# Optimization experiments

Measured on AMD Instinct MI355X. Metric: run time of the kernel, lower is better.

Reference implementation:

```python
import jax, jax.numpy as jnp
import numpy as np

B, ME, R, N, HSZ, V, L, NHEADS = 32, 384, 128, 512, 500, 1000, 2, 4


def _ln(x, g, b, eps=1e-5):
    mu = jnp.mean(x, axis=-1, keepdims=True)
    var = jnp.mean((x - mu) ** 2, axis=-1, keepdims=True)
    return (x - mu) / jnp.sqrt(var + eps) * g + b


def setup_inputs() -> dict:
    key = jax.random.key(0)
    ks = jax.random.split(key, 12)
    ent_vec = jax.random.normal(ks[0], (B, ME, HSZ), jnp.float32)
    entity_num = jax.random.randint(ks[1], (B,), 1, ME + 1)
    rels = jax.random.randint(ks[2], (B, R), 0, V)
    sizes = entity_num + R  # real graph size per sample (<= N)
    idx = jnp.arange(N)
    valid = idx[None, :] < sizes[:, None]
    adj = jax.random.uniform(ks[3], (B, N, N)) < 0.3
    adj = adj & valid[:, None, :] & valid[:, :, None]
    adj = adj | jnp.eye(N, dtype=bool)[None]  # keep diagonal so no all-masked row
    adj = adj.astype(jnp.int32)
    rel_embed = jax.random.normal(ks[4], (V, HSZ)) * (2.0 / (V + HSZ)) ** 0.5  # xavier_normal

    def w(k, shape):
        return (jax.random.normal(k, shape) * 0.03).astype(jnp.float32)

    Wq = w(ks[5], (L, HSZ, HSZ)); Wk = w(ks[6], (L, HSZ, HSZ))
    Wv = w(ks[7], (L, HSZ, HSZ)); Wo = w(ks[8], (L, HSZ, HSZ))
    W1 = w(ks[9], (L, HSZ, 4 * HSZ)); W2 = w(ks[10], (L, 4 * HSZ, HSZ))
    zH = jnp.zeros((L, HSZ), jnp.float32)
    return dict(
        ent_vec=ent_vec, entity_num=entity_num, rels=rels, adj=adj,
        rel_embed=rel_embed,
        Wq=Wq, bq=zH, Wk=Wk, bk=zH, Wv=Wv, bv=zH, Wo=Wo, bo=zH,
        W1=W1, b1=jnp.zeros((L, 4 * HSZ), jnp.float32), W2=W2, b2=zH,
        ln1_g=jnp.ones((L, HSZ), jnp.float32), ln1_b=zH,
        ln2_g=jnp.ones((L, HSZ), jnp.float32), ln2_b=zH,
        prelu_a=jnp.full((L, 4 * HSZ), 0.25, jnp.float32),
    )


def reference(ent_vec, entity_num, rels, adj, rel_embed,
              Wq, bq, Wk, bk, Wv, bv, Wo, bo,
              W1, b1, W2, b2, ln1_g, ln1_b, ln2_g, ln2_b, prelu_a):
    Bb, Me, H = ent_vec.shape
    Rr = rels.shape[1]
    Nn = adj.shape[1]
    Ll = Wq.shape[0]
    dh = H // NHEADS
    idx = jnp.arange(Nn)

    # query_graph = concat(ent_vec[i][:entity_num[i]], rel_embed(rels[i])), padded to N
    is_ent = idx[None, :] < entity_num[:, None]
    eidx = jnp.minimum(idx[None, :], Me - 1)
    ent_part = jnp.take_along_axis(ent_vec, eidx[:, :, None], axis=1)  # (B,N,H)
    ridx = jnp.clip(idx[None, :] - entity_num[:, None], 0, Rr - 1)
    rel_ids = jnp.take_along_axis(rels, ridx, axis=1)  # (B,N)
    rel_part = rel_embed[rel_ids]  # (B,N,H)
    nodes = jnp.where(is_ent[:, :, None], ent_part, rel_part)
    sizes = entity_num + Rr
    validm = idx[None, :] < sizes[:, None]
    nodes = nodes * validm[:, :, None]

    attn_mask = adj != 0  # original masks where adj == 0
    scale = 1.0 / jnp.sqrt(jnp.float32(dh))
    for l in range(Ll):
        kv = jax.lax.stop_gradient(nodes)  # key_graph is detached in original
        q = (nodes @ Wq[l] + bq[l]).reshape(Bb, Nn, NHEADS, dh)
        k = (kv @ Wk[l] + bk[l]).reshape(Bb, Nn, NHEADS, dh)
        v = (kv @ Wv[l] + bv[l]).reshape(Bb, Nn, NHEADS, dh)
        s = jnp.einsum('bqhd,bkhd->bhqk', q, k) * scale
        s = jnp.where(attn_mask[:, None], s, jnp.float32(-1e9))
        a = jax.nn.softmax(s, axis=-1)
        ctx = jnp.einsum('bhqk,bkhd->bqhd', a, v).reshape(Bb, Nn, H)
        o = ctx @ Wo[l] + bo[l]
        t = _ln(o, ln1_g[l], ln1_b[l])
        h1 = t @ W1[l] + b1[l]
        h1 = jnp.where(h1 > 0, h1, prelu_a[l] * h1)  # PReLU, per-channel
        f = h1 @ W2[l] + b2[l]
        nodes = _ln(f + t, ln2_g[l], ln2_b[l])

    node_emb = nodes * validm[:, :, None]  # original pads graphs with zeros
    gidx = jnp.broadcast_to(entity_num[:, None, None], (Bb, 1, H))
    glob = jnp.take_along_axis(nodes, gidx, axis=1)[:, 0]  # query_graph[entity_num[i]]
    out_mask = idx[None, :] <= sizes[:, None]  # faithful '<=' as in original
    return glob, node_emb, out_mask
```

## Files before the change

### kernel.cpp

```cpp
#include <hip/hip_runtime.h>

#define BB 32
#define MEE 384
#define RRELS 128
#define NNODES 512
#define HSZ 500
#define DHEAD 125
#define NHEADS_ 4
#define HID 2000
#define NLAYER 2

#define KP 512
#define HIDP 2048

typedef unsigned short ushort_t;
typedef __attribute__((ext_vector_type(8))) short bf16x8;
typedef __attribute__((ext_vector_type(4))) float f32x4;
typedef __attribute__((ext_vector_type(4))) short s16x4;

static __device__ __forceinline__ unsigned short f2bf(float x) {
    unsigned u = __float_as_uint(x);
    u = u + 0x7fff + ((u >> 16) & 1);
    return (unsigned short)(u >> 16);
}
static __device__ __forceinline__ float bf2f(unsigned short b) {
    return __uint_as_float((unsigned)b << 16);
}

static __device__ __forceinline__ void gload_lds16(const ushort_t* g, ushort_t* l) {
    __builtin_amdgcn_global_load_lds(
        (const __attribute__((address_space(1))) void*)g,
        (__attribute__((address_space(3))) void*)l, 16, 0, 0);
}

__global__ __launch_bounds__(256) void build_nodes_k(
    const float* __restrict__ ent_vec, const int* __restrict__ entity_num,
    const int* __restrict__ rels, const float* __restrict__ rel_embed,
    ushort_t* __restrict__ xb)
{
    int b = blockIdx.x / NNODES;
    int n = blockIdx.x % NNODES;
    int e = entity_num[b];
    const float* src = nullptr;
    if (n < e)               src = ent_vec + ((size_t)b * MEE + n) * HSZ;
    else if (n < e + RRELS)  src = rel_embed + (size_t)rels[b * RRELS + (n - e)] * HSZ;
    ushort_t* xd = xb + ((size_t)b * NNODES + n) * KP;
    for (int d = threadIdx.x; d < KP; d += 256)
        xd[d] = (src && d < HSZ) ? f2bf(src[d]) : 0;
}

__global__ __launch_bounds__(256) void adj_bits_k(
    const int* __restrict__ adj, unsigned int* __restrict__ bits)
{
    int gw = (blockIdx.x * 256 + threadIdx.x) >> 6;
    int lane = threadIdx.x & 63;
    int v = adj[(size_t)gw * 64 + lane];
    unsigned long long mk = __ballot(v != 0);
    if (lane == 0)  bits[gw * 2]     = (unsigned int)mk;
    if (lane == 32) bits[gw * 2 + 1] = (unsigned int)(mk >> 32);
}

__global__ __launch_bounds__(256) void wcvt_t_k(
    const float* __restrict__ pWq, const float* __restrict__ pWk,
    const float* __restrict__ pWv, const float* __restrict__ pWo,
    const float* __restrict__ pW1, const float* __restrict__ pW2,
    ushort_t* __restrict__ wqkv, ushort_t* __restrict__ wo,
    ushort_t* __restrict__ w1, ushort_t* __restrict__ w2)
{
    __shared__ float T[64][65];
    int blk = blockIdx.x;
    const float* W; ushort_t* out; int Kr, Nr, Kpp, tt;
    if (blk < 192)      { int s = blk >> 6; W = s == 0 ? pWq : (s == 1 ? pWk : pWv);
                          out = wqkv + s * 262144; Kr = 500; Nr = 500; Kpp = 512; tt = blk & 63; }
    else if (blk < 256) { W = pWo; out = wo;  Kr = 500;  Nr = 500;  Kpp = 512;  tt = blk - 192; }
    else if (blk < 512) { W = pW1; out = w1;  Kr = 500;  Nr = 2000; Kpp = 512;  tt = blk - 256; }
    else                { W = pW2; out = w2;  Kr = 2000; Nr = 500;  Kpp = 2048; tt = blk - 512; }
    int ntk = Kpp >> 6;
    int tk = tt % ntk, tn = tt / ntk;
    int tid = threadIdx.x;
#pragma unroll
    for (int p = 0; p < 4; ++p) {
        int kl = p * 16 + (tid >> 4);
        int k  = tk * 64 + kl;
        int nl = (tid & 15) * 4;
        int n  = tn * 64 + nl;
        float4 v = make_float4(0.f, 0.f, 0.f, 0.f);
        if (k < Kr) {
            if (n + 3 < Nr) v = *(const float4*)&W[(size_t)k * Nr + n];
            else {
                if (n     < Nr) v.x = W[(size_t)k * Nr + n];
                if (n + 1 < Nr) v.y = W[(size_t)k * Nr + n + 1];
                if (n + 2 < Nr) v.z = W[(size_t)k * Nr + n + 2];
                if (n + 3 < Nr) v.w = W[(size_t)k * Nr + n + 3];
            }
        }
        T[kl][nl] = v.x; T[kl][nl + 1] = v.y; T[kl][nl + 2] = v.z; T[kl][nl + 3] = v.w;
    }
    __syncthreads();
#pragma unroll
    for (int p = 0; p < 2; ++p) {
        int nl  = p * 32 + (tid >> 3);
        int kl8 = (tid & 7) * 8;
        bf16x8 o;
#pragma unroll
        for (int j = 0; j < 8; ++j) o[j] = (short)f2bf(T[kl8 + j][nl]);
        *(bf16x8*)&out[(size_t)(tn * 64 + nl) * Kpp + tk * 64 + kl8] = o;
    }
}

__global__ __launch_bounds__(256, 2) void gemm_mfma_k(
    const ushort_t* __restrict__ A, const ushort_t* __restrict__ Bt,
    const float* __restrict__ bias0, const float* __restrict__ bias1,
    const float* __restrict__ bias2,
    ushort_t* __restrict__ outB, ushort_t* __restrict__ outK,
    ushort_t* __restrict__ outV,
    int M, int Np, int Kp, int Nreal,
    const float* __restrict__ prelu, int mode)
{
    __shared__ ushort_t Al[2][128 * 32];
    __shared__ ushort_t Bl[2][128 * 32];

    const int nwg = gridDim.x * gridDim.y;
    const int bid = blockIdx.y * gridDim.x + blockIdx.x;
    const int swz = (bid & 7) * (nwg >> 3) + (bid >> 3);
    const int bm = (swz / gridDim.x) * 128;
    const int bn = (swz % gridDim.x) * 128;

    const int tid = threadIdx.x;
    const int wid = tid >> 6, lane = tid & 63;
    const int wr = wid >> 1, wc = wid & 1;
    const int lr = lane & 15, lk = lane >> 4;

    f32x4 acc[4][4];
#pragma unroll
    for (int i = 0; i < 4; ++i)
#pragma unroll
        for (int j = 0; j < 4; ++j)
#pragma unroll
            for (int r = 0; r < 4; ++r) acc[i][j][r] = 0.f;

    const int srow = tid >> 2;
    const int skseg = (tid & 3) * 8;
    const ushort_t* Ag0 = A + (size_t)(bm + srow) * Kp + skseg;
    const ushort_t* Ag1 = A + (size_t)(bm + 64 + srow) * Kp + skseg;
    const ushort_t* Bg0 = Bt + (size_t)(bn + srow) * Kp + skseg;
    const ushort_t* Bg1 = Bt + (size_t)(bn + 64 + srow) * Kp + skseg;

    auto stage = [&](int bi, int k0) {
        gload_lds16(Ag0 + k0, &Al[bi][wid * 512]);
        gload_lds16(Ag1 + k0, &Al[bi][2048 + wid * 512]);
        gload_lds16(Bg0 + k0, &Bl[bi][wid * 512]);
        gload_lds16(Bg1 + k0, &Bl[bi][2048 + wid * 512]);
    };

    stage(0, 0);
    __syncthreads();
    int cur = 0;

    for (int k0 = 0; k0 < Kp; k0 += 32) {
        if (k0 + 32 < Kp) stage(cur ^ 1, k0 + 32);

        bf16x8 af[4], bfr[4];
#pragma unroll
        for (int mi = 0; mi < 4; ++mi)
            af[mi] = *(const bf16x8*)&Al[cur][(wr * 64 + mi * 16 + lr) * 32 + lk * 8];
#pragma unroll
        for (int ni = 0; ni < 4; ++ni)
            bfr[ni] = *(const bf16x8*)&Bl[cur][(wc * 64 + ni * 16 + lr) * 32 + lk * 8];
        __builtin_amdgcn_s_setprio(1);
#pragma unroll
        for (int mi = 0; mi < 4; ++mi)
#pragma unroll
            for (int ni = 0; ni < 4; ++ni)
                acc[mi][ni] = __builtin_amdgcn_mfma_f32_16x16x32_bf16(
                    af[mi], bfr[ni], acc[mi][ni], 0, 0, 0);
        __builtin_amdgcn_s_setprio(0);

        __syncthreads();
        cur ^= 1;
    }

    if (mode == 1) {
#pragma unroll
        for (int ni = 0; ni < 4; ++ni) {
            int col = bn + wc * 64 + ni * 16 + lr;
            int reg = col >> 9, c = col & 511;
            bool cok = c < 500;
            int hh, dh;
            if (cok) { hh = c / 125; dh = c - hh * 125; }
            else     { hh = (c - 500) / 3; dh = 125 + (c - 500) % 3; }
            const float* bp = reg == 0 ? bias0 : (reg == 1 ? bias1 : bias2);
            float bv = cok ? bp[c] : 0.f;
#pragma unroll
            for (int mi = 0; mi < 4; ++mi) {
                int row0 = bm + wr * 64 + mi * 16 + lk * 4;
                int b_ = row0 >> 9, n0 = row0 & 511;
                size_t bh = (size_t)b_ * 4 + hh;
                if (reg == 2) {
                    s16x4 pk;
#pragma unroll
                    for (int r = 0; r < 4; ++r) {
                        float val = acc[mi][ni][r] + bv;
                        pk[r] = cok ? (short)f2bf(val) : (short)0;
                    }
                    *(s16x4*)&outV[(bh * 128 + dh) * 512 + n0] = pk;
                } else {
                    ushort_t* dst = reg == 0 ? outB : outK;
#pragma unroll
                    for (int r = 0; r < 4; ++r) {
                        float val = acc[mi][ni][r] + bv;
                        dst[(bh * 512 + n0 + r) * 128 + dh] = cok ? f2bf(val) : 0;
                    }
                }
            }
        }
    } else {
#pragma unroll
        for (int ni = 0; ni < 4; ++ni) {
            int col = bn + wc * 64 + ni * 16 + lr;
            bool cok = col < Nreal;
            float bv = cok ? bias0[col] : 0.f;
            float pv = (prelu && cok) ? prelu[col] : 0.f;
#pragma unroll
            for (int mi = 0; mi < 4; ++mi) {
                int row0 = bm + wr * 64 + mi * 16 + lk * 4;
#pragma unroll
                for (int r = 0; r < 4; ++r) {
                    int row = row0 + r;
                    float val = acc[mi][ni][r] + bv;
                    if (prelu) val = val > 0.f ? val : pv * val;
                    outB[(size_t)row * Np + col] = cok ? f2bf(val) : 0;
                }
            }
        }
    }
}

#define KTT 64
__global__ __launch_bounds__(256, 2) void attn_mfma_k(
    const ushort_t* __restrict__ qh, const ushort_t* __restrict__ kh,
    const ushort_t* __restrict__ vT, const unsigned int* __restrict__ abits,
    ushort_t* __restrict__ ctxb)
{
    __shared__ ushort_t Kl[2][KTT * 128];
    __shared__ ushort_t Vl[2][128 * KTT];
    __shared__ ushort_t Pl[4][32 * KTT];

    const int bid = blockIdx.x;
    const int wg = (bid & 7) * 64 + (bid >> 3);
    const int qt2 = wg & 3, bh = wg >> 2;
    const int b = bh >> 2, h = bh & 3;
    const int tid = threadIdx.x, wid = tid >> 6, lane = tid & 63;
    const int lr = lane & 15, lk = lane >> 4;
    const int q0 = qt2 * 128 + wid * 32;
    const float scale = 0.08944271909999159f;

    bf16x8 qa[2][4];
#pragma unroll
    for (int t = 0; t < 2; ++t) {
        const ushort_t* qbase = qh + ((size_t)bh * 512 + q0 + t * 16 + lr) * 128;
#pragma unroll
        for (int ks = 0; ks < 4; ++ks)
            qa[t][ks] = *(const bf16x8*)&qbase[ks * 32 + lk * 8];
    }

    f32x4 accO[2][8];
#pragma unroll
    for (int t = 0; t < 2; ++t)
#pragma unroll
        for (int i = 0; i < 8; ++i)
#pragma unroll
            for (int r = 0; r < 4; ++r) accO[t][i][r] = 0.f;
    float m_[2][4], l_[2][4];
#pragma unroll
    for (int t = 0; t < 2; ++t)
#pragma unroll
        for (int r = 0; r < 4; ++r) { m_[t][r] = -3e38f; l_[t][r] = 0.f; }

    const unsigned int* ab = abits + ((size_t)b * NNODES + q0) * 16;

    auto stage = [&](int bi, int kt) {
#pragma unroll
        for (int i = 0; i < 4; ++i) {
            int linear = (wid * 4 + i) * 64 + lane;
            int row = linear >> 4, cc = linear & 15;
            int cs = cc ^ (row & 7);
            gload_lds16(kh + ((size_t)bh * 512 + kt * 64 + row) * 128 + cs * 8,
                        &Kl[bi][(wid * 4 + i) * 512]);
        }
#pragma unroll
        for (int i = 0; i < 4; ++i) {
            int linear = (wid * 4 + i) * 64 + lane;
            int row = linear >> 3, cc = linear & 7;
            int cs = cc ^ (row & 7);
            gload_lds16(vT + ((size_t)bh * 128 + row) * 512 + kt * 64 + cs * 8,
                        &Vl[bi][(wid * 4 + i) * 512]);
        }
    };

    stage(0, 0);
    __syncthreads();
    int cur = 0;

    for (int kt = 0; kt < NNODES / KTT; ++kt) {
        if (kt < NNODES / KTT - 1) stage(cur ^ 1, kt + 1);

        unsigned int mw[2][4][2];
#pragma unroll
        for (int t = 0; t < 2; ++t)
#pragma unroll
            for (int r = 0; r < 4; ++r) {
                int qrow = t * 16 + lk * 4 + r;
                mw[t][r][0] = ab[qrow * 16 + kt * 2];
                mw[t][r][1] = ab[qrow * 16 + kt * 2 + 1];
            }

#pragma unroll
        for (int t = 0; t < 2; ++t) {
            f32x4 accS[4];
#pragma unroll
            for (int ni = 0; ni < 4; ++ni)
#pragma unroll
                for (int r = 0; r < 4; ++r) accS[ni][r] = 0.f;
            __builtin_amdgcn_s_setprio(1);
#pragma unroll
            for (int ks = 0; ks < 4; ++ks) {
#pragma unroll
                for (int ni = 0; ni < 4; ++ni) {
                    int row = ni * 16 + lr;
                    int ch = (ks * 4 + lk) ^ (row & 7);
                    bf16x8 kb = *(const bf16x8*)&Kl[cur][row * 128 + ch * 8];
                    accS[ni] = __builtin_amdgcn_mfma_f32_16x16x32_bf16(
                        qa[t][ks], kb, accS[ni], 0, 0, 0);
                }
            }
            __builtin_amdgcn_s_setprio(0);
#pragma unroll
            for (int r = 0; r < 4; ++r) {
                float s[4];
#pragma unroll
                for (int ni = 0; ni < 4; ++ni) {
                    unsigned int word = mw[t][r][ni >> 1];
                    int bit = (ni & 1) * 16 + lr;
                    bool on = (word >> bit) & 1u;
                    s[ni] = on ? accS[ni][r] * scale : -1e9f;
                }
                float rowmax = fmaxf(fmaxf(s[0], s[1]), fmaxf(s[2], s[3]));
                rowmax = fmaxf(rowmax, __shfl_xor(rowmax, 1));
                rowmax = fmaxf(rowmax, __shfl_xor(rowmax, 2));
                rowmax = fmaxf(rowmax, __shfl_xor(rowmax, 4));
                rowmax = fmaxf(rowmax, __shfl_xor(rowmax, 8));
                float mnew = fmaxf(m_[t][r], rowmax);
                float f = __expf(m_[t][r] - mnew);
                m_[t][r] = mnew;
                float p[4], rs = 0.f;
#pragma unroll
                for (int ni = 0; ni < 4; ++ni) { p[ni] = __expf(s[ni] - mnew); rs += p[ni]; }
                rs += __shfl_xor(rs, 1);
                rs += __shfl_xor(rs, 2);
                rs += __shfl_xor(rs, 4);
                rs += __shfl_xor(rs, 8);
                l_[t][r] = l_[t][r] * f + rs;
#pragma unroll
                for (int di = 0; di < 8; ++di) accO[t][di][r] *= f;
                int q = t * 16 + lk * 4 + r;
#pragma unroll
                for (int ni = 0; ni < 4; ++ni) {
                    int key = ni * 16 + lr;
                    Pl[wid][q * 64 + (((key >> 3) ^ (q & 7)) << 3) + (key & 7)] = f2bf(p[ni]);
                }
            }
        }

#pragma unroll
        for (int t = 0; t < 2; ++t) {
#pragma unroll
            for (int ksp = 0; ksp < 2; ++ksp) {
                int q = t * 16 + lr;
                int k0p = ksp * 32 + lk * 8;
                bf16x8 pa = *(const bf16x8*)&Pl[wid][q * 64 + (((k0p >> 3) ^ (q & 7)) << 3)];
                __builtin_amdgcn_s_setprio(1);
#pragma unroll
                for (int di = 0; di < 8; ++di) {
                    int row = di * 16 + lr;
                    int ch = (ksp * 4 + lk) ^ (row & 7);
                    bf16x8 vb = *(const bf16x8*)&Vl[cur][row * 64 + ch * 8];
                    accO[t][di] = __builtin_amdgcn_mfma_f32_16x16x32_bf16(
                        pa, vb, accO[t][di], 0, 0, 0);
                }
                __builtin_amdgcn_s_setprio(0);
            }
        }
        __syncthreads();
        cur ^= 1;
    }

    float inv[2][4];
#pragma unroll
    for (int t = 0; t < 2; ++t)
#pragma unroll
        for (int r = 0; r < 4; ++r) inv[t][r] = 1.f / l_[t][r];
#pragma unroll
    for (int t = 0; t < 2; ++t)
#pragma unroll
        for (int di = 0; di < 8; ++di) {
            int d = di * 16 + lr;
            if (d < DHEAD) {
#pragma unroll
                for (int r = 0; r < 4; ++r) {
                    int qg = q0 + t * 16 + lk * 4 + r;
                    ctxb[((size_t)b * NNODES + qg) * KP + h * DHEAD + d] =
                        f2bf(accO[t][di][r] * inv[t][r]);
                }
            }
        }
    if (h == 3) {
        int row = q0 + (lane & 31);
        int c0 = 500 + (lane >> 5) * 6;
#pragma unroll
        for (int j = 0; j < 6; ++j)
            ctxb[((size_t)b * NNODES + row) * KP + c0 + j] = 0;
    }
}

__global__ __launch_bounds__(256) void ln_k(
    const ushort_t* __restrict__ x, const ushort_t* __restrict__ res,
    const float* __restrict__ g, const float* __restrict__ bta,
    ushort_t* __restrict__ outB)
{
    size_t row = blockIdx.x;
    const unsigned int* xr = (const unsigned int*)(x + row * KP);
    const unsigned int* rr = res ? (const unsigned int*)(res + row * KP) : nullptr;
    int t = threadIdx.x;
    int d0 = 2 * t;
    unsigned int xv = xr[t];
    float v0 = bf2f((unsigned short)(xv & 0xffff));
    float v1 = bf2f((unsigned short)(xv >> 16));
    if (rr) {
        unsigned int rv = rr[t];
        v0 += bf2f((unsigned short)(rv & 0xffff));
        v1 += bf2f((unsigned short)(rv >> 16));
    }
    if (d0 >= HSZ) v0 = 0.f;
    if (d0 + 1 >= HSZ) v1 = 0.f;
    float s = v0 + v1, s2 = v0 * v0 + v1 * v1;

    __shared__ float red[8];
    int wave = t >> 6, lane = t & 63;
    for (int o = 1; o < 64; o <<= 1) { s += __shfl_xor(s, o); s2 += __shfl_xor(s2, o); }
    if (lane == 0) { red[wave] = s; red[4 + wave] = s2; }
    __syncthreads();
    s  = red[0] + red[1] + red[2] + red[3];
    s2 = red[4] + red[5] + red[6] + red[7];
    float mean = s / HSZ;
    float var  = s2 / HSZ - mean * mean;
    float rstd = rsqrtf(var + 1e-5f);

    float o0 = 0.f, o1 = 0.f;
    if (d0 < HSZ)     o0 = (v0 - mean) * rstd * g[d0] + bta[d0];
    if (d0 + 1 < HSZ) o1 = (v1 - mean) * rstd * g[d0 + 1] + bta[d0 + 1];
    unsigned int pk = (unsigned int)f2bf(o0) | ((unsigned int)f2bf(o1) << 16);
    if (d0 >= HSZ) pk = 0;
    else if (d0 + 1 >= HSZ) pk = (unsigned int)f2bf(o0);
    ((unsigned int*)(outB + row * KP))[t] = pk;
}

__global__ __launch_bounds__(256) void finalize_k(
    const ushort_t* __restrict__ nodes, const int* __restrict__ entity_num,
    float* __restrict__ out)
{
    int b = blockIdx.x / NNODES;
    int n = blockIdx.x % NNODES;
    int e = entity_num[b];
    int size = e + RRELS;
    const ushort_t* src = nodes + ((size_t)b * NNODES + n) * KP;
    float* ne = out + (size_t)BB * HSZ + ((size_t)b * NNODES + n) * HSZ;
    bool valid = n < size;
    for (int d = threadIdx.x; d < HSZ; d += 256) ne[d] = valid ? bf2f(src[d]) : 0.f;
    if (n == e) {
        float* gl = out + (size_t)b * HSZ;
        for (int d = threadIdx.x; d < HSZ; d += 256) gl[d] = bf2f(src[d]);
    }
    if (threadIdx.x == 0) {
        out[(size_t)BB * HSZ + (size_t)BB * NNODES * HSZ + (size_t)b * NNODES + n] =
            (n <= size) ? 1.f : 0.f;
    }
}

extern "C" void kernel_launch(void* const* d_in, const int* in_sizes, int n_in,
                              void* d_out, int out_size, void* d_ws, size_t ws_size,
                              hipStream_t stream)
{
    const float* ent_vec    = (const float*)d_in[0];
    const int*   entity_num = (const int*)d_in[1];
    const int*   rels       = (const int*)d_in[2];
    const int*   adj        = (const int*)d_in[3];
    const float* rel_embed  = (const float*)d_in[4];
    const float* Wq = (const float*)d_in[5],  *bq = (const float*)d_in[6];
    const float* Wk = (const float*)d_in[7],  *bk = (const float*)d_in[8];
    const float* Wv = (const float*)d_in[9],  *bv = (const float*)d_in[10];
    const float* Wo = (const float*)d_in[11], *bo = (const float*)d_in[12];
    const float* W1 = (const float*)d_in[13], *b1 = (const float*)d_in[14];
    const float* W2 = (const float*)d_in[15], *b2 = (const float*)d_in[16];
    const float* ln1g = (const float*)d_in[17], *ln1b = (const float*)d_in[18];
    const float* ln2g = (const float*)d_in[19], *ln2b = (const float*)d_in[20];
    const float* pa = (const float*)d_in[21];

    const int M = BB * NNODES;
    const size_t SP = (size_t)M * KP;

    ushort_t* Xb   = (ushort_t*)d_ws;
    ushort_t* ctxb = Xb + SP;
    ushort_t* tb   = ctxb + SP;
    ushort_t* ob   = tb + SP;
    ushort_t* fb   = ob + SP;
    ushort_t* h1b  = fb + SP;
    ushort_t* wqkvb = h1b + (size_t)M * HIDP;
    ushort_t* wob  = wqkvb + 3 * KP * KP;
    ushort_t* w1b  = wob + KP * KP;
    ushort_t* w2b  = w1b + (size_t)HIDP * KP;

    ushort_t* qh  = h1b;
    ushort_t* kh  = h1b + SP;
    ushort_t* vTb = h1b + 2 * SP;

    unsigned int* abits = (unsigned int*)d_out;

    build_nodes_k<<<BB * NNODES, 256, 0, stream>>>(ent_vec, entity_num, rels, rel_embed, Xb);
    adj_bits_k<<<(BB * NNODES * NNODES) / 64 / 4, 256, 0, stream>>>(adj, abits);

    for (int l = 0; l < NLAYER; ++l) {
        const float* bq_l = bq + (size_t)l * HSZ;
        const float* bk_l = bk + (size_t)l * HSZ;
        const float* bv_l = bv + (size_t)l * HSZ;
        const float* bo_l = bo + (size_t)l * HSZ;
        const float* b1_l = b1 + (size_t)l * HID;
        const float* b2_l = b2 + (size_t)l * HSZ;
        const float* pa_l = pa + (size_t)l * HID;

        wcvt_t_k<<<768, 256, 0, stream>>>(
            Wq + (size_t)l * HSZ * HSZ, Wk + (size_t)l * HSZ * HSZ,
            Wv + (size_t)l * HSZ * HSZ, Wo + (size_t)l * HSZ * HSZ,
            W1 + (size_t)l * HSZ * HID, W2 + (size_t)l * HID * HSZ,
            wqkvb, wob, w1b, w2b);

        dim3 gQKV(1536 / 128, M / 128);
        gemm_mfma_k<<<gQKV, 256, 0, stream>>>(Xb, wqkvb, bq_l, bk_l, bv_l,
                                              qh, kh, vTb,
                                              M, 1536, KP, HSZ, nullptr, 1);

        attn_mfma_k<<<BB * NHEADS_ * 4, 256, 0, stream>>>(qh, kh, vTb, abits, ctxb);

        dim3 gO(KP / 128, M / 128);
        gemm_mfma_k<<<gO, 256, 0, stream>>>(ctxb, wob, bo_l, nullptr, nullptr,
                                            ob, nullptr, nullptr,
                                            M, KP, KP, HSZ, nullptr, 0);
        ln_k<<<M, 256, 0, stream>>>(ob, nullptr,
                                    ln1g + (size_t)l * HSZ, ln1b + (size_t)l * HSZ,
                                    tb);

        dim3 g1(HIDP / 128, M / 128);
        gemm_mfma_k<<<g1, 256, 0, stream>>>(tb, w1b, b1_l, nullptr, nullptr,
                                            h1b, nullptr, nullptr,
                                            M, HIDP, KP, HID, pa_l, 0);
        dim3 g2(KP / 128, M / 128);
        gemm_mfma_k<<<g2, 256, 0, stream>>>(h1b, w2b, b2_l, nullptr, nullptr,
                                            fb, nullptr, nullptr,
                                            M, KP, HIDP, HSZ, nullptr, 0);

        ln_k<<<M, 256, 0, stream>>>(fb, tb,
                                    ln2g + (size_t)l * HSZ, ln2b + (size_t)l * HSZ,
                                    Xb);
    }

    finalize_k<<<BB * NNODES, 256, 0, stream>>>(Xb, entity_num, (float*)d_out);
}
```

Baseline: 530.7 us.

## Use lazy softmax rescaling with exp2 in attention and fuse finalize into last LayerNorm

The attention kernel folds log2(e) into the score scale, switches to exp2f, and rescales the output accumulator and row sum only when some row max in the wave grows by more than 8, which skips the per-tile rescale work most of the time. Separately, the final LayerNorm now writes the fp32 outputs, the global vector and the mask directly, which removes the separate finalize kernel and its extra read of the node tensor. The lazy rescale relies on the fp32 accumulators tolerating exponent growth of up to 2^8. Final outputs also now come from fp32 LayerNorm values instead of bf16-rounded ones.

```diff
diff --git a/kernel.cpp b/kernel.cpp
--- a/kernel.cpp
+++ b/kernel.cpp
@@ -253,7 +253,7 @@
     const int tid = threadIdx.x, wid = tid >> 6, lane = tid & 63;
     const int lr = lane & 15, lk = lane >> 4;
     const int q0 = qt2 * 128 + wid * 32;
-    const float scale = 0.08944271909999159f;
+    const float scale2 = 0.08944271909999159f * 1.44269504088896f;
 
     bf16x8 qa[2][4];
 #pragma unroll
@@ -335,34 +335,52 @@
                 }
             }
             __builtin_amdgcn_s_setprio(0);
+
+            float s_all[4][4], mnew[4];
 #pragma unroll
             for (int r = 0; r < 4; ++r) {
-                float s[4];
+                float rowmax = -3e38f;
 #pragma unroll
                 for (int ni = 0; ni < 4; ++ni) {
                     unsigned int word = mw[t][r][ni >> 1];
                     int bit = (ni & 1) * 16 + lr;
                     bool on = (word >> bit) & 1u;
-                    s[ni] = on ? accS[ni][r] * scale : -1e9f;
-                }
-                float rowmax = fmaxf(fmaxf(s[0], s[1]), fmaxf(s[2], s[3]));
+                    float sv = on ? accS[ni][r] * scale2 : -1e9f;
+                    s_all[r][ni] = sv;
+                    rowmax = fmaxf(rowmax, sv);
+                }
                 rowmax = fmaxf(rowmax, __shfl_xor(rowmax, 1));
                 rowmax = fmaxf(rowmax, __shfl_xor(rowmax, 2));
                 rowmax = fmaxf(rowmax, __shfl_xor(rowmax, 4));
                 rowmax = fmaxf(rowmax, __shfl_xor(rowmax, 8));
-                float mnew = fmaxf(m_[t][r], rowmax);
-                float f = __expf(m_[t][r] - mnew);
-                m_[t][r] = mnew;
+                mnew[r] = fmaxf(m_[t][r], rowmax);
+            }
+            bool need = false;
+#pragma unroll
+            for (int r = 0; r < 4; ++r) need = need || (mnew[r] - m_[t][r] > 8.f);
+            if (__any(need)) {
+#pragma unroll
+                for (int r = 0; r < 4; ++r) {
+                    float f = exp2f(m_[t][r] - mnew[r]);
+                    m_[t][r] = mnew[r];
+                    l_[t][r] *= f;
+#pragma unroll
+                    for (int di = 0; di < 8; ++di) accO[t][di][r] *= f;
+                }
+            }
+#pragma unroll
+            for (int r = 0; r < 4; ++r) {
                 float p[4], rs = 0.f;
 #pragma unroll
-                for (int ni = 0; ni < 4; ++ni) { p[ni] = __expf(s[ni] - mnew); rs += p[ni]; }
+                for (int ni = 0; ni < 4; ++ni) {
+                    p[ni] = exp2f(s_all[r][ni] - m_[t][r]);
+                    rs += p[ni];
+                }
                 rs += __shfl_xor(rs, 1);
                 rs += __shfl_xor(rs, 2);
                 rs += __shfl_xor(rs, 4);
                 rs += __shfl_xor(rs, 8);
-                l_[t][r] = l_[t][r] * f + rs;
-#pragma unroll
-                for (int di = 0; di < 8; ++di) accO[t][di][r] *= f;
+                l_[t][r] += rs;
                 int q = t * 16 + lk * 4 + r;
 #pragma unroll
                 for (int ni = 0; ni < 4; ++ni) {
@@ -426,7 +444,8 @@
 __global__ __launch_bounds__(256) void ln_k(
     const ushort_t* __restrict__ x, const ushort_t* __restrict__ res,
     const float* __restrict__ g, const float* __restrict__ bta,
-    ushort_t* __restrict__ outB)
+    ushort_t* __restrict__ outB,
+    const int* __restrict__ entity_num, float* __restrict__ out, int final_)
 {
     size_t row = blockIdx.x;
     const unsigned int* xr = (const unsigned int*)(x + row * KP);
@@ -459,31 +478,28 @@
     float o0 = 0.f, o1 = 0.f;
     if (d0 < HSZ)     o0 = (v0 - mean) * rstd * g[d0] + bta[d0];
     if (d0 + 1 < HSZ) o1 = (v1 - mean) * rstd * g[d0 + 1] + bta[d0 + 1];
-    unsigned int pk = (unsigned int)f2bf(o0) | ((unsigned int)f2bf(o1) << 16);
-    if (d0 >= HSZ) pk = 0;
-    else if (d0 + 1 >= HSZ) pk = (unsigned int)f2bf(o0);
-    ((unsigned int*)(outB + row * KP))[t] = pk;
-}
-
-__global__ __launch_bounds__(256) void finalize_k(
-    const ushort_t* __restrict__ nodes, const int* __restrict__ entity_num,
-    float* __restrict__ out)
-{
-    int b = blockIdx.x / NNODES;
-    int n = blockIdx.x % NNODES;
-    int e = entity_num[b];
-    int size = e + RRELS;
-    const ushort_t* src = nodes + ((size_t)b * NNODES + n) * KP;
-    float* ne = out + (size_t)BB * HSZ + ((size_t)b * NNODES + n) * HSZ;
-    bool valid = n < size;
-    for (int d = threadIdx.x; d < HSZ; d += 256) ne[d] = valid ? bf2f(src[d]) : 0.f;
-    if (n == e) {
-        float* gl = out + (size_t)b * HSZ;
-        for (int d = threadIdx.x; d < HSZ; d += 256) gl[d] = bf2f(src[d]);
-    }
-    if (threadIdx.x == 0) {
-        out[(size_t)BB * HSZ + (size_t)BB * NNODES * HSZ + (size_t)b * NNODES + n] =
-            (n <= size) ? 1.f : 0.f;
+
+    if (!final_) {
+        unsigned int pk = (unsigned int)f2bf(o0) | ((unsigned int)f2bf(o1) << 16);
+        if (d0 >= HSZ) pk = 0;
+        else if (d0 + 1 >= HSZ) pk = (unsigned int)f2bf(o0);
+        ((unsigned int*)(outB + row * KP))[t] = pk;
+    } else {
+        int b = (int)(row >> 9), n = (int)(row & 511);
+        int e = entity_num[b];
+        int size = e + RRELS;
+        bool valid = n < size;
+        float* ne = out + (size_t)BB * HSZ + row * HSZ;
+        if (d0 < HSZ)     ne[d0]     = valid ? o0 : 0.f;
+        if (d0 + 1 < HSZ) ne[d0 + 1] = valid ? o1 : 0.f;
+        if (n == e) {
+            float* gl = out + (size_t)b * HSZ;
+            if (d0 < HSZ)     gl[d0]     = o0;
+            if (d0 + 1 < HSZ) gl[d0 + 1] = o1;
+        }
+        if (t == 0)
+            out[(size_t)BB * HSZ + (size_t)BB * NNODES * HSZ + row] =
+                (n <= size) ? 1.f : 0.f;
     }
 }
 
@@ -557,7 +573,7 @@
                                             M, KP, KP, HSZ, nullptr, 0);
         ln_k<<<M, 256, 0, stream>>>(ob, nullptr,
                                     ln1g + (size_t)l * HSZ, ln1b + (size_t)l * HSZ,
-                                    tb);
+                                    tb, nullptr, nullptr, 0);
 
         dim3 g1(HIDP / 128, M / 128);
         gemm_mfma_k<<<g1, 256, 0, stream>>>(tb, w1b, b1_l, nullptr, nullptr,
@@ -568,10 +584,9 @@
                                             fb, nullptr, nullptr,
                                             M, KP, HIDP, HSZ, nullptr, 0);
 
+        int fin = (l == NLAYER - 1) ? 1 : 0;
         ln_k<<<M, 256, 0, stream>>>(fb, tb,
                                     ln2g + (size_t)l * HSZ, ln2b + (size_t)l * HSZ,
-                                    Xb);
-    }
-
-    finalize_k<<<BB * NNODES, 256, 0, stream>>>(Xb, entity_num, (float*)d_out);
-}
+                                    Xb, entity_num, (float*)d_out, fin);
+    }
+}
```

After: 529.0 us. Within noise of the previous version (-0.3%).
